# Optimization experiments

Measured on AMD Instinct MI355X. Metric: run time of the kernel, lower is better.

Reference implementation:

```python
import jax, jax.numpy as jnp
import numpy as np

B, C, H, W = 4, 192, 64, 64
D_STATE, D_CONV, EXPAND = 16, 4, 2
DIN = EXPAND * C            # 384
DT_RANK = (C + 15) // 16    # 12
EPS = 1e-5


def _silu(v):
    return v * jax.nn.sigmoid(v)


def _snake(x2d):
    # x2d: [B, H, W, D]; reverse every odd row (boustrophedon / snake scan).
    # This op is its own inverse.
    odd = (jnp.arange(x2d.shape[1]) % 2 == 1)[None, :, None, None]
    return jnp.where(odd, jnp.flip(x2d, axis=2), x2d)


def setup_inputs() -> dict:
    key = jax.random.key(0)
    ks = jax.random.split(key, 12)
    s = lambda k, shape, sc: jax.random.normal(k, shape, dtype=jnp.float32) * sc
    inp = {
        "x": jax.random.normal(ks[0], (B, C, H, W), dtype=jnp.float32),
        "gn_gamma": jnp.ones((C,), jnp.float32),
        "gn_beta": jnp.zeros((C,), jnp.float32),
        "in_proj_w": s(ks[1], (2 * DIN, C), 0.05),
        "conv1d_w": s(ks[2], (DIN, D_CONV), 0.2),
        "conv1d_b": jnp.zeros((DIN,), jnp.float32),
        "x_proj_w": s(ks[3], (DT_RANK + 2 * D_STATE, DIN), 0.05),
        "dt_proj_w": s(ks[4], (DIN, DT_RANK), 0.1),
        "dt_proj_b": s(ks[5], (DIN,), 0.1),
        "A_log": jnp.log(jnp.broadcast_to(jnp.arange(1, D_STATE + 1, dtype=jnp.float32), (DIN, D_STATE))),
        "Dskip": jnp.ones((DIN,), jnp.float32),
        "le_w": s(ks[6], (DIN, 1, 3, 3), 0.1),      # depthwise 3x3 local enhancement
        "out_proj_w": s(ks[7], (C, DIN), 0.05),
        "proj_out_w": s(ks[8], (C, C), 0.05),        # 1x1 conv, no bias
    }
    return inp


def reference(x, gn_gamma, gn_beta, in_proj_w, conv1d_w, conv1d_b,
              x_proj_w, dt_proj_w, dt_proj_b, A_log, Dskip, le_w,
              out_proj_w, proj_out_w):
    b, c, h, w = x.shape
    L = h * w
    din = DIN

    # GroupNorm(1, C): normalize over (C, H, W) per sample
    mu = jnp.mean(x, axis=(1, 2, 3), keepdims=True)
    var = jnp.var(x, axis=(1, 2, 3), keepdims=True)
    xn = (x - mu) * jax.lax.rsqrt(var + EPS)
    xn = xn * gn_gamma[None, :, None, None] + gn_beta[None, :, None, None]

    xs = xn.reshape(b, c, L).transpose(0, 2, 1)            # [B, L, C]

    # input projection -> (u, z)
    xz = jnp.einsum('blc,dc->bld', xs, in_proj_w)          # [B, L, 2*din]
    u, z = jnp.split(xz, 2, axis=-1)

    # snake scan ordering on u
    u = _snake(u.reshape(b, h, w, din)).reshape(b, L, din)

    # causal depthwise conv1d along sequence + SiLU
    u_t = u.transpose(0, 2, 1)                              # [B, din, L]
    u_c = jax.lax.conv_general_dilated(
        u_t, conv1d_w[:, None, :], (1,), [(D_CONV - 1, 0)],
        feature_group_count=din)
    u_c = _silu(u_c + conv1d_b[None, :, None]).transpose(0, 2, 1)  # [B, L, din]

    # input-dependent SSM parameters
    dbl = jnp.einsum('bld,ed->ble', u_c, x_proj_w)          # [B, L, dt_rank+2N]
    dt, Bm, Cm = jnp.split(dbl, [DT_RANK, DT_RANK + D_STATE], axis=-1)
    delta = jax.nn.softplus(jnp.einsum('blr,dr->bld', dt, dt_proj_w) + dt_proj_b)
    A = -jnp.exp(A_log)                                     # [din, N]

    # selective scan over L steps, carry state [B, din, N]
    def step(hc, inp):
        d_t, B_t, C_t, u_t_ = inp                           # [B,din],[B,N],[B,N],[B,din]
        dA = jnp.exp(d_t[..., None] * A)                    # [B, din, N]
        hc = dA * hc + (d_t * u_t_)[..., None] * B_t[:, None, :]
        y_t = jnp.einsum('bdn,bn->bd', hc, C_t)
        return hc, y_t

    h0 = jnp.zeros((b, din, D_STATE), delta.dtype)
    xs_scan = (delta.transpose(1, 0, 2), Bm.transpose(1, 0, 2),
               Cm.transpose(1, 0, 2), u_c.transpose(1, 0, 2))
    _, ys = jax.lax.scan(step, h0, xs_scan)                 # ys: [L, B, din]
    y = ys.transpose(1, 0, 2) + u_c * Dskip                 # [B, L, din]

    # undo snake ordering (involution), then gate with z (raster order)
    y = _snake(y.reshape(b, h, w, din)).reshape(b, L, din)
    y = y * _silu(z)

    # local enhancement: depthwise 3x3 conv residual on the 2D map
    y2d = y.reshape(b, h, w, din).transpose(0, 3, 1, 2)     # [B, din, H, W]
    y_le = jax.lax.conv_general_dilated(
        y2d, le_w, (1, 1), [(1, 1), (1, 1)], feature_group_count=din)
    y = y + y_le.transpose(0, 2, 3, 1).reshape(b, L, din)

    # output projection back to C, reshape, then 1x1 conv
    out_seq = jnp.einsum('bld,cd->blc', y, out_proj_w)      # [B, L, C]
    out = out_seq.transpose(0, 2, 1).reshape(b, c, h, w)
    out = jnp.einsum('bchw,oc->bohw', out, proj_out_w)
    return out
```

## Files before the change

kernel.cpp:

```cpp
#include <hip/hip_runtime.h>
#include <cstddef>

constexpr int CB  = 4;
constexpr int CC  = 192;
constexpr int CH  = 64;
constexpr int CW  = 64;
constexpr int CL  = CH * CW;
constexpr int DIN = 384;
constexpr int NST = 16;
constexpr int DTR = 12;

constexpr int NCHUNK = 64;
constexpr int NELEM  = CB * DIN * NST;

constexpr int WS_PART  = 0;
constexpr int WS_STAT  = 512;
constexpr int WS_BFIN  = 1024;
constexpr int WS_BFOUT = WS_BFIN + 73728;
constexpr int WS_BFPO  = WS_BFOUT + 36864;
constexpr int WS_BFXF  = WS_BFPO + 18432;
constexpr int WS_LWT   = WS_BFXF + 86016;
constexpr int WS_BIG   = WS_LWT + 3456;
constexpr size_t NBL   = (size_t)CB * CL;
constexpr size_t BIGSZ = NBL * DIN;

using half8 = __attribute__((ext_vector_type(8))) _Float16;
using half4 = __attribute__((ext_vector_type(4))) _Float16;
using f32x4 = __attribute__((ext_vector_type(4))) float;

__device__ __forceinline__ float sigm(float v) { return 1.f / (1.f + __expf(-v)); }
__device__ __forceinline__ float silu_f(float v) { return v * sigm(v); }
__device__ __forceinline__ float softplus_f(float v) { return v > 20.f ? v : log1pf(__expf(v)); }
template <int PAT>
__device__ __forceinline__ float quadswz(float v) {
  return __int_as_float(__builtin_amdgcn_ds_swizzle(__float_as_int(v), PAT));
}

__global__ __launch_bounds__(256) void gn_partial(const float* __restrict__ x,
                                                  float* __restrict__ part) {
  int b = blockIdx.x >> 6;
  int chunk = blockIdx.x & 63;
  const float* px = x + (size_t)b * CC * CL + (size_t)chunk * 12288;
  float s = 0.f, s2 = 0.f;
  for (int i = threadIdx.x; i < 12288 / 4; i += 256) {
    float4 v = ((const float4*)px)[i];
    s  += v.x + v.y + v.z + v.w;
    s2 += v.x * v.x + v.y * v.y + v.z * v.z + v.w * v.w;
  }
  __shared__ float ls[4], ls2[4];
  for (int off = 32; off; off >>= 1) { s += __shfl_down(s, off); s2 += __shfl_down(s2, off); }
  int wid = threadIdx.x >> 6, lane = threadIdx.x & 63;
  if (lane == 0) { ls[wid] = s; ls2[wid] = s2; }
  __syncthreads();
  if (threadIdx.x == 0) {
    float t = 0.f, t2 = 0.f;
    for (int i = 0; i < 4; i++) { t += ls[i]; t2 += ls2[i]; }
    part[blockIdx.x * 2] = t;
    part[blockIdx.x * 2 + 1] = t2;
  }
}

__global__ __launch_bounds__(256) void gn_final(const float* __restrict__ part,
                                                float* __restrict__ stat) {
  int b = threadIdx.x >> 6;
  int i = threadIdx.x & 63;
  float s = part[(b * 64 + i) * 2];
  float s2 = part[(b * 64 + i) * 2 + 1];
  for (int off = 32; off; off >>= 1) { s += __shfl_down(s, off); s2 += __shfl_down(s2, off); }
  if (i == 0) {
    float n = (float)(CC * CL);
    float mu = s / n;
    float var = s2 / n - mu * mu;
    stat[b * 2] = mu;
    stat[b * 2 + 1] = rsqrtf(var + 1e-5f);
  }
}

__device__ __forceinline__ void pack_frag(_Float16* dst, int idx, int KS,
                                          const float* __restrict__ W, int KDIM) {
  int j = idx & 7, lane = (idx >> 3) & 63, colq = (idx >> 9) & 3, rest = idx >> 11;
  int ks = rest % KS, nt = rest / KS;
  int col = nt * 64 + colq * 16 + (lane & 15);
  int k = ks * 32 + ((lane >> 4) << 3) + j;
  dst[idx] = (_Float16)W[(size_t)col * KDIM + k];
}

__device__ __forceinline__ void pack_xf(_Float16* dst, int idx,
                                        const float* __restrict__ xw,
                                        const float* __restrict__ dtw) {
  int j = idx & 7, lane = (idx >> 3) & 63, colq = (idx >> 9) & 3, rest = idx >> 11;
  int ks = rest % 12, nt = rest / 12;
  int col = nt * 64 + colq * 16 + (lane & 15);
  int k = ks * 32 + ((lane >> 4) << 3) + j;
  float v = 0.f;
  if (col < 384) {
#pragma unroll
    for (int r = 0; r < 12; r++)
      v += xw[r * 384 + k] * dtw[col * 12 + r];
  } else if (col < 416) {
    v = xw[(col - 384 + 12) * 384 + k];
  }
  dst[idx] = (_Float16)v;
}

__global__ __launch_bounds__(256) void transpose_all(
    const float* __restrict__ in_proj_w, const float* __restrict__ x_proj_w,
    const float* __restrict__ dt_proj_w, const float* __restrict__ out_proj_w,
    const float* __restrict__ proj_out_w, const float* __restrict__ le_w,
    float* __restrict__ ws) {
  int idx = blockIdx.x * 256 + threadIdx.x;
  if (idx < 147456) {
    pack_frag((_Float16*)(ws + WS_BFIN), idx, 6, in_proj_w, 192);
    return;
  }
  idx -= 147456;
  if (idx < 73728) {
    pack_frag((_Float16*)(ws + WS_BFOUT), idx, 12, out_proj_w, 384);
    return;
  }
  idx -= 73728;
  if (idx < 36864) {
    pack_frag((_Float16*)(ws + WS_BFPO), idx, 6, proj_out_w, 192);
    return;
  }
  idx -= 36864;
  if (idx < 172032) {
    pack_xf((_Float16*)(ws + WS_BFXF), idx, x_proj_w, dt_proj_w);
    return;
  }
  idx -= 172032;
  if (idx < 3456) {
    int t9 = idx / 384, d = idx % 384;
    ws[WS_LWT + idx] = le_w[d * 9 + t9];
  }
}

__global__ __launch_bounds__(256) void gemm_inproj_mfma(
    const float* __restrict__ x, const _Float16* __restrict__ Bf,
    const float* __restrict__ stat, const float* __restrict__ gamma,
    const float* __restrict__ beta, float* __restrict__ u, float* __restrict__ z) {
  int mt = blockIdx.x & 255, nt = blockIdx.x >> 8;
  int m0 = mt * 64;
  int b = m0 >> 12, l0 = m0 & 4095;
  float mu = stat[b * 2], rs = stat[b * 2 + 1];
  __shared__ __align__(16) _Float16 Ah[64][200];
  int tid = threadIdx.x;
  int row = tid & 63, cq = tid >> 6;
#pragma unroll
  for (int i = 0; i < 12; i++) {
    int c0 = cq * 4 + i * 16;
    half4 h;
#pragma unroll
    for (int cc = 0; cc < 4; cc++) {
      int c = c0 + cc;
      float g = gamma[c] * rs;
      float bt = beta[c] - mu * g;
      float xv = x[((size_t)(b * 192 + c) << 12) + l0 + row];
      h[cc] = (_Float16)(xv * g + bt);
    }
    *(half4*)&Ah[row][c0] = h;
  }
  __syncthreads();
  int w = tid >> 6, lane = tid & 63;
  int wm = (w >> 1) * 32, wcol = w & 1;
  int r16 = lane & 15, kg = lane >> 4;
  f32x4 acc[2][2] = {};
#pragma unroll
  for (int ks = 0; ks < 6; ks++) {
    half8 a0 = *(const half8*)&Ah[wm + r16][ks * 32 + kg * 8];
    half8 a1 = *(const half8*)&Ah[wm + 16 + r16][ks * 32 + kg * 8];
    half8 b0 = *(const half8*)&Bf[(((size_t)(nt * 6 + ks) * 4 + wcol * 2 + 0) << 9) + lane * 8];
    half8 b1 = *(const half8*)&Bf[(((size_t)(nt * 6 + ks) * 4 + wcol * 2 + 1) << 9) + lane * 8];
    acc[0][0] = __builtin_amdgcn_mfma_f32_16x16x32_f16(a0, b0, acc[0][0], 0, 0, 0);
    acc[0][1] = __builtin_amdgcn_mfma_f32_16x16x32_f16(a0, b1, acc[0][1], 0, 0, 0);
    acc[1][0] = __builtin_amdgcn_mfma_f32_16x16x32_f16(a1, b0, acc[1][0], 0, 0, 0);
    acc[1][1] = __builtin_amdgcn_mfma_f32_16x16x32_f16(a1, b1, acc[1][1], 0, 0, 0);
  }
  int hrow = l0 >> 6;
  bool odd = hrow & 1;
#pragma unroll
  for (int mi = 0; mi < 2; mi++)
#pragma unroll
    for (int ni = 0; ni < 2; ni++)
#pragma unroll
      for (int r = 0; r < 4; r++) {
        int wloc = wm + mi * 16 + kg * 4 + r;
        int d = nt * 64 + wcol * 32 + ni * 16 + r16;
        float val = acc[mi][ni][r];
        if (d < DIN) {
          int ls = odd ? (hrow << 6) + 63 - wloc : l0 + wloc;
          u[((size_t)(b << 12) + ls) * DIN + d] = val;
        } else {
          z[((size_t)(b << 12) + l0 + wloc) * DIN + (d - DIN)] = val;
        }
      }
}

template <int KDIM, int NDIM, bool TRANSOUT>
__global__ __launch_bounds__(256) void gemm_mfma(
    const float* __restrict__ A, const _Float16* __restrict__ Bf,
    float* __restrict__ C) {
  constexpr int KS = KDIM / 32;
  int mt = blockIdx.x & 255, nt = blockIdx.x >> 8;
  int m0 = mt * 64, n0 = nt * 64;
  __shared__ __align__(16) _Float16 Ah[64][KDIM + 8];
  int tid = threadIdx.x;
  {
    int r16s = tid >> 4, kq = tid & 15;
#pragma unroll
    for (int rr = 0; rr < 4; rr++) {
      int rowi = r16s + rr * 16;
#pragma unroll
      for (int kk = 0; kk < KDIM / 64; kk++) {
        float4 v = *(const float4*)&A[(size_t)(m0 + rowi) * KDIM + kk * 64 + kq * 4];
        half4 h;
        h[0] = (_Float16)v.x; h[1] = (_Float16)v.y;
        h[2] = (_Float16)v.z; h[3] = (_Float16)v.w;
        *(half4*)&Ah[rowi][kk * 64 + kq * 4] = h;
      }
    }
  }
  __syncthreads();
  int w = tid >> 6, lane = tid & 63;
  int wm = (w >> 1) * 32, wcol = w & 1;
  int r16 = lane & 15, kg = lane >> 4;
  f32x4 acc[2][2] = {};
#pragma unroll
  for (int ks = 0; ks < KS; ks++) {
    half8 a0 = *(const half8*)&Ah[wm + r16][ks * 32 + kg * 8];
    half8 a1 = *(const half8*)&Ah[wm + 16 + r16][ks * 32 + kg * 8];
    half8 b0 = *(const half8*)&Bf[(((size_t)(nt * KS + ks) * 4 + wcol * 2 + 0) << 9) + lane * 8];
    half8 b1 = *(const half8*)&Bf[(((size_t)(nt * KS + ks) * 4 + wcol * 2 + 1) << 9) + lane * 8];
    acc[0][0] = __builtin_amdgcn_mfma_f32_16x16x32_f16(a0, b0, acc[0][0], 0, 0, 0);
    acc[0][1] = __builtin_amdgcn_mfma_f32_16x16x32_f16(a0, b1, acc[0][1], 0, 0, 0);
    acc[1][0] = __builtin_amdgcn_mfma_f32_16x16x32_f16(a1, b0, acc[1][0], 0, 0, 0);
    acc[1][1] = __builtin_amdgcn_mfma_f32_16x16x32_f16(a1, b1, acc[1][1], 0, 0, 0);
  }
  if constexpr (!TRANSOUT) {
#pragma unroll
    for (int mi = 0; mi < 2; mi++)
#pragma unroll
      for (int ni = 0; ni < 2; ni++)
#pragma unroll
        for (int r = 0; r < 4; r++) {
          int rowo = wm + mi * 16 + kg * 4 + r;
          int col = wcol * 32 + ni * 16 + r16;
          C[(size_t)(m0 + rowo) * NDIM + n0 + col] = acc[mi][ni][r];
        }
  } else {
    __shared__ float Cs[64][68];
#pragma unroll
    for (int mi = 0; mi < 2; mi++)
#pragma unroll
      for (int ni = 0; ni < 2; ni++)
#pragma unroll
        for (int r = 0; r < 4; r++)
          Cs[wcol * 32 + ni * 16 + r16][wm + mi * 16 + kg * 4 + r] = acc[mi][ni][r];
    __syncthreads();
    int b = m0 >> 12, l0 = m0 & 4095;
    int li = tid & 63;
#pragma unroll
    for (int rr = 0; rr < 16; rr++) {
      int o = rr * 4 + (tid >> 6);
      C[(size_t)(b * CC + n0 + o) * CL + l0 + li] = Cs[o][li];
    }
  }
}

__global__ __launch_bounds__(256) void xfull_gemm(
    const float* __restrict__ uc, const _Float16* __restrict__ Bf,
    const float* __restrict__ dt_bias, float* __restrict__ delta,
    float* __restrict__ Bmb, float* __restrict__ Cmb) {
  int mt = blockIdx.x & 255, nt = blockIdx.x >> 8;
  int m0 = mt * 64;
  __shared__ __align__(16) _Float16 Ah[64][392];
  int tid = threadIdx.x;
  {
    int r16s = tid >> 4, kq = tid & 15;
#pragma unroll
    for (int rr = 0; rr < 4; rr++) {
      int rowi = r16s + rr * 16;
#pragma unroll
      for (int kk = 0; kk < 6; kk++) {
        float4 v = *(const float4*)&uc[(size_t)(m0 + rowi) * DIN + kk * 64 + kq * 4];
        half4 h;
        h[0] = (_Float16)v.x; h[1] = (_Float16)v.y;
        h[2] = (_Float16)v.z; h[3] = (_Float16)v.w;
        *(half4*)&Ah[rowi][kk * 64 + kq * 4] = h;
      }
    }
  }
  __syncthreads();
  int w = tid >> 6, lane = tid & 63;
  int wm = (w >> 1) * 32, wcol = w & 1;
  int r16 = lane & 15, kg = lane >> 4;
  f32x4 acc[2][2] = {};
#pragma unroll
  for (int ks = 0; ks < 12; ks++) {
    half8 a0 = *(const half8*)&Ah[wm + r16][ks * 32 + kg * 8];
    half8 a1 = *(const half8*)&Ah[wm + 16 + r16][ks * 32 + kg * 8];
    half8 b0 = *(const half8*)&Bf[(((size_t)(nt * 12 + ks) * 4 + wcol * 2 + 0) << 9) + lane * 8];
    half8 b1 = *(const half8*)&Bf[(((size_t)(nt * 12 + ks) * 4 + wcol * 2 + 1) << 9) + lane * 8];
    acc[0][0] = __builtin_amdgcn_mfma_f32_16x16x32_f16(a0, b0, acc[0][0], 0, 0, 0);
    acc[0][1] = __builtin_amdgcn_mfma_f32_16x16x32_f16(a0, b1, acc[0][1], 0, 0, 0);
    acc[1][0] = __builtin_amdgcn_mfma_f32_16x16x32_f16(a1, b0, acc[1][0], 0, 0, 0);
    acc[1][1] = __builtin_amdgcn_mfma_f32_16x16x32_f16(a1, b1, acc[1][1], 0, 0, 0);
  }
#pragma unroll
  for (int mi = 0; mi < 2; mi++)
#pragma unroll
    for (int ni = 0; ni < 2; ni++)
#pragma unroll
      for (int r = 0; r < 4; r++) {
        size_t m = m0 + wm + mi * 16 + kg * 4 + r;
        int gc = nt * 64 + wcol * 32 + ni * 16 + r16;
        float val = acc[mi][ni][r];
        if (gc < 384)
          delta[m * DIN + gc] = softplus_f(val + dt_bias[gc]);
        else if (gc < 400)
          Bmb[m * 16 + (gc - 384)] = val;
        else if (gc < 416)
          Cmb[m * 16 + (gc - 400)] = val;
      }
}

__global__ __launch_bounds__(256) void conv_silu_tiled(
    const float* __restrict__ u, const float* __restrict__ cw,
    const float* __restrict__ cb, float* __restrict__ uc) {
  int bid = blockIdx.x;
  int dg = bid % 6;
  int lt = (bid / 6) % 64;
  int b  = bid / (6 * 64);
  int d0 = dg * 64;
  int l0 = lt * 64;
  __shared__ float S[67][68];
  int t = threadIdx.x;
  for (int idx = t; idx < 67 * 16; idx += 256) {
    int row = idx >> 4, c4i = idx & 15;
    int l = l0 + row - 3;
    float4 v = make_float4(0.f, 0.f, 0.f, 0.f);
    if (l >= 0)
      v = *(const float4*)&u[((size_t)((b << 12) + l)) * DIN + d0 + c4i * 4];
    *(float4*)&S[row][c4i * 4] = v;
  }
  __syncthreads();
  int c4 = t & 15, j0 = (t >> 4) << 2;
  int dd = d0 + c4 * 4;
  float4 cwv[4];
#pragma unroll
  for (int i = 0; i < 4; i++) cwv[i] = *(const float4*)&cw[(dd + i) * 4];
  float4 bias = *(const float4*)&cb[dd];
  float4 win[7];
#pragma unroll
  for (int k = 0; k < 7; k++) win[k] = *(float4*)&S[j0 + k][c4 * 4];
#pragma unroll
  for (int j = 0; j < 4; j++) {
    float4 acc = bias;
#pragma unroll
    for (int k = 0; k < 4; k++) {
      float4 v = win[j + k];
      acc.x = fmaf(v.x, ((const float*)&cwv[0])[k], acc.x);
      acc.y = fmaf(v.y, ((const float*)&cwv[1])[k], acc.y);
      acc.z = fmaf(v.z, ((const float*)&cwv[2])[k], acc.z);
      acc.w = fmaf(v.w, ((const float*)&cwv[3])[k], acc.w);
    }
    acc.x = silu_f(acc.x);
    acc.y = silu_f(acc.y);
    acc.z = silu_f(acc.z);
    acc.w = silu_f(acc.w);
    *(float4*)&uc[((size_t)((b << 12) + l0 + j0 + j)) * DIN + dd] = acc;
  }
}

__global__ __launch_bounds__(256) void scan_partial(
    const float* __restrict__ delta, const float* __restrict__ uc,
    const float* __restrict__ Bmb, const float* __restrict__ A_log,
    float* __restrict__ hend, float* __restrict__ Pbuf) {
  int bid = blockIdx.x;
  int chunk = bid & 63, bg = bid >> 6;
  int b = bg / 6, g = bg % 6;
  int t = threadIdx.x;
  int dloc = t >> 2, q = t & 3;
  int d = g * 64 + dloc;
  __shared__ float sD[64][64], sU[64][64], sB[64][16];
  size_t baseBL = ((size_t)b << 12) + chunk * 64;
  {
    int row = t >> 2, cg = (t & 3) * 16;
    const float* dp = &delta[(baseBL + row) * DIN + g * 64 + cg];
    const float* up = &uc[(baseBL + row) * DIN + g * 64 + cg];
#pragma unroll
    for (int c = 0; c < 4; c++) {
      *(float4*)&sD[row][cg + 4 * c] = *(const float4*)&dp[4 * c];
      *(float4*)&sU[row][cg + 4 * c] = *(const float4*)&up[4 * c];
    }
    *(float4*)&sB[row][q * 4] = *(const float4*)&Bmb[(baseBL + row) * 16 + q * 4];
  }
  __syncthreads();
  float4 av = *(const float4*)&A_log[d * 16 + 4 * q];
  float a0 = -__expf(av.x), a1 = -__expf(av.y), a2 = -__expf(av.z), a3 = -__expf(av.w);
  float h0 = 0.f, h1 = 0.f, h2 = 0.f, h3 = 0.f, sdel = 0.f;
#pragma unroll 8
  for (int ll = 0; ll < 64; ll++) {
    float dv = sD[ll][dloc];
    float uv = sU[ll][dloc];
    float4 Bv = *(const float4*)&sB[ll][q * 4];
    float duv = dv * uv;
    h0 = fmaf(__expf(dv * a0), h0, duv * Bv.x);
    h1 = fmaf(__expf(dv * a1), h1, duv * Bv.y);
    h2 = fmaf(__expf(dv * a2), h2, duv * Bv.z);
    h3 = fmaf(__expf(dv * a3), h3, duv * Bv.w);
    sdel += dv;
  }
  size_t e = ((size_t)(b * DIN + d)) * 16 + 4 * q;
  float4 hv; hv.x = h0; hv.y = h1; hv.z = h2; hv.w = h3;
  *(float4*)&hend[(size_t)chunk * NELEM + e] = hv;
  float4 pv;
  pv.x = __expf(a0 * sdel); pv.y = __expf(a1 * sdel);
  pv.z = __expf(a2 * sdel); pv.w = __expf(a3 * sdel);
  *(float4*)&Pbuf[(size_t)chunk * NELEM + e] = pv;
}

__global__ __launch_bounds__(256) void scan_combine(
    const float* __restrict__ hend, const float* __restrict__ Pbuf,
    float* __restrict__ hin) {
  int e = blockIdx.x * 256 + threadIdx.x;
  float h = 0.f;
  float Pc = Pbuf[e], Hc = hend[e];
#pragma unroll 8
  for (int c = 0; c < NCHUNK; c++) {
    float Pn = 0.f, Hn = 0.f;
    if (c < NCHUNK - 1) {
      Pn = Pbuf[(size_t)(c + 1) * NELEM + e];
      Hn = hend[(size_t)(c + 1) * NELEM + e];
    }
    hin[(size_t)c * NELEM + e] = h;
    h = fmaf(Pc, h, Hc);
    Pc = Pn; Hc = Hn;
  }
}

__global__ __launch_bounds__(256) void scan_final(
    const float* __restrict__ delta, const float* __restrict__ uc,
    const float* __restrict__ Bmb, const float* __restrict__ Cmb,
    const float* __restrict__ A_log, const float* __restrict__ Dskip,
    const float* __restrict__ z, const float* __restrict__ hin,
    float* __restrict__ yr) {
  int bid = blockIdx.x;
  int chunk = bid & 63, bg = bid >> 6;
  int b = bg / 6, g = bg % 6;
  int t = threadIdx.x;
  int dloc = t >> 2, q = t & 3;
  int d = g * 64 + dloc;
  __shared__ float sD[64][64], sU[64][64], sB[64][16], sC[64][16];
  size_t baseBL = ((size_t)b << 12) + chunk * 64;
  {
    int row = t >> 2, cg = (t & 3) * 16;
    const float* dp = &delta[(baseBL + row) * DIN + g * 64 + cg];
    const float* up = &uc[(baseBL + row) * DIN + g * 64 + cg];
#pragma unroll
    for (int c = 0; c < 4; c++) {
      *(float4*)&sD[row][cg + 4 * c] = *(const float4*)&dp[4 * c];
      *(float4*)&sU[row][cg + 4 * c] = *(const float4*)&up[4 * c];
    }
    *(float4*)&sB[row][q * 4] = *(const float4*)&Bmb[(baseBL + row) * 16 + q * 4];
    *(float4*)&sC[row][q * 4] = *(const float4*)&Cmb[(baseBL + row) * 16 + q * 4];
  }
  __syncthreads();
  float4 av = *(const float4*)&A_log[d * 16 + 4 * q];
  float a0 = -__expf(av.x), a1 = -__expf(av.y), a2 = -__expf(av.z), a3 = -__expf(av.w);
  size_t e = ((size_t)(b * DIN + d)) * 16 + 4 * q;
  float4 hv = *(const float4*)&hin[(size_t)chunk * NELEM + e];
  float h0 = hv.x, h1 = hv.y, h2 = hv.z, h3 = hv.w;
  float yk[16];
#pragma unroll
  for (int ll = 0; ll < 64; ll++) {
    float dv = sD[ll][dloc];
    float uv = sU[ll][dloc];
    float4 Bv = *(const float4*)&sB[ll][q * 4];
    float4 Cv = *(const float4*)&sC[ll][q * 4];
    float duv = dv * uv;
    h0 = fmaf(__expf(dv * a0), h0, duv * Bv.x);
    h1 = fmaf(__expf(dv * a1), h1, duv * Bv.y);
    h2 = fmaf(__expf(dv * a2), h2, duv * Bv.z);
    h3 = fmaf(__expf(dv * a3), h3, duv * Bv.w);
    float yp = h0 * Cv.x + h1 * Cv.y + h2 * Cv.z + h3 * Cv.w;
    yp += quadswz<0x041F>(yp);
    yp += quadswz<0x081F>(yp);
    if ((ll & 3) == q) yk[ll >> 2] = yp;
  }
  float dsk = Dskip[d];
  bool odd = chunk & 1;
#pragma unroll
  for (int i = 0; i < 16; i++) {
    int ll = 4 * i + q;
    int wr = odd ? 63 - ll : ll;
    size_t ro = baseBL + wr;
    float uvll = sU[ll][dloc];
    float zv = z[ro * DIN + d];
    yr[ro * DIN + d] = (yk[i] + uvll * dsk) * silu_f(zv);
  }
}

__global__ __launch_bounds__(256) void le_conv_tiled(
    const float* __restrict__ yr, const float* __restrict__ lwT,
    float* __restrict__ y2) {
  int bid = blockIdx.x;
  int dg = bid % 24;
  int ht = (bid / 24) % 16;
  int b  = bid / (24 * 16);
  int d0 = dg * 16;
  int h0 = ht * 4;
  __shared__ float S[6][66][20];
  int t = threadIdx.x;
  int dq = t & 3, w = t >> 2;
#pragma unroll
  for (int r = 0; r < 6; r++) {
    int hh = h0 - 1 + r;
    float4 v = make_float4(0.f, 0.f, 0.f, 0.f);
    if (hh >= 0 && hh < 64)
      v = *(const float4*)&yr[((size_t)((b << 12) + (hh << 6) + w)) * DIN + d0 + dq * 4];
    *(float4*)&S[r][w + 1][dq * 4] = v;
    if (w == 0)  *(float4*)&S[r][0][dq * 4]  = make_float4(0.f, 0.f, 0.f, 0.f);
    if (w == 63) *(float4*)&S[r][65][dq * 4] = make_float4(0.f, 0.f, 0.f, 0.f);
  }
  __syncthreads();
  float4 wv[9];
#pragma unroll
  for (int i = 0; i < 9; i++)
    wv[i] = *(const float4*)&lwT[i * DIN + d0 + dq * 4];
#pragma unroll
  for (int hr = 0; hr < 4; hr++) {
    float4 acc = *(float4*)&S[hr + 1][w + 1][dq * 4];
#pragma unroll
    for (int ki = 0; ki < 3; ki++)
#pragma unroll
      for (int kj = 0; kj < 3; kj++) {
        float4 v = *(float4*)&S[hr + ki][w + kj][dq * 4];
        float4 c = wv[ki * 3 + kj];
        acc.x = fmaf(v.x, c.x, acc.x);
        acc.y = fmaf(v.y, c.y, acc.y);
        acc.z = fmaf(v.z, c.z, acc.z);
        acc.w = fmaf(v.w, c.w, acc.w);
      }
    int l = ((h0 + hr) << 6) + w;
    *(float4*)&y2[((size_t)((b << 12) + l)) * DIN + d0 + dq * 4] = acc;
  }
}

extern "C" void kernel_launch(void* const* d_in, const int* in_sizes, int n_in,
                              void* d_out, int out_size, void* d_ws, size_t ws_size,
                              hipStream_t stream) {
  const float* x          = (const float*)d_in[0];
  const float* gn_gamma   = (const float*)d_in[1];
  const float* gn_beta    = (const float*)d_in[2];
  const float* in_proj_w  = (const float*)d_in[3];
  const float* conv1d_w   = (const float*)d_in[4];
  const float* conv1d_b   = (const float*)d_in[5];
  const float* x_proj_w   = (const float*)d_in[6];
  const float* dt_proj_w  = (const float*)d_in[7];
  const float* dt_proj_b  = (const float*)d_in[8];
  const float* A_log      = (const float*)d_in[9];
  const float* Dskip      = (const float*)d_in[10];
  const float* le_w       = (const float*)d_in[11];
  const float* out_proj_w = (const float*)d_in[12];
  const float* proj_out_w = (const float*)d_in[13];
  float* out = (float*)d_out;

  float* ws      = (float*)d_ws;
  float* part    = ws + WS_PART;
  float* stat    = ws + WS_STAT;
  _Float16* BfIn  = (_Float16*)(ws + WS_BFIN);
  _Float16* BfOut = (_Float16*)(ws + WS_BFOUT);
  _Float16* BfPo  = (_Float16*)(ws + WS_BFPO);
  _Float16* BfXf  = (_Float16*)(ws + WS_BFXF);
  float* lwT    = ws + WS_LWT;
  float* u      = ws + WS_BIG;
  float* zb     = u + BIGSZ;
  float* uc     = zb + BIGSZ;
  float* delta  = uc + BIGSZ;
  float* yr     = delta + BIGSZ;
  float* Bmb    = yr + BIGSZ;
  float* Cmb    = Bmb + NBL * NST;
  float* y2     = uc;
  float* outseq = u;
  float* hend   = u;
  float* Pbuf   = u + (size_t)NCHUNK * NELEM;
  float* hin    = u + 2 * (size_t)NCHUNK * NELEM;

  gn_partial<<<256, 256, 0, stream>>>(x, part);
  gn_final<<<1, 256, 0, stream>>>(part, stat);
  transpose_all<<<1694, 256, 0, stream>>>(in_proj_w, x_proj_w, dt_proj_w,
                                          out_proj_w, proj_out_w, le_w, ws);
  gemm_inproj_mfma<<<256 * 12, 256, 0, stream>>>(x, BfIn, stat, gn_gamma, gn_beta, u, zb);
  conv_silu_tiled<<<1536, 256, 0, stream>>>(u, conv1d_w, conv1d_b, uc);
  xfull_gemm<<<256 * 7, 256, 0, stream>>>(uc, BfXf, dt_proj_b, delta, Bmb, Cmb);
  scan_partial<<<1536, 256, 0, stream>>>(delta, uc, Bmb, A_log, hend, Pbuf);
  scan_combine<<<96, 256, 0, stream>>>(hend, Pbuf, hin);
  scan_final<<<1536, 256, 0, stream>>>(delta, uc, Bmb, Cmb, A_log, Dskip,
                                       zb, hin, yr);
  le_conv_tiled<<<1536, 256, 0, stream>>>(yr, lwT, y2);
  gemm_mfma<384, 192, false><<<256 * 3, 256, 0, stream>>>(y2, BfOut, outseq);
  gemm_mfma<192, 192, true><<<256 * 3, 256, 0, stream>>>(outseq, BfPo, out);
}
```

Measured before the change: 269.9 us.

## Emit fp16 MFMA-fragment-layout activations from producers and feed GEMMs directly

The conv_silu and local-enhancement kernels now write fp16 copies of their outputs laid out in the MFMA A-fragment order. The x_proj, out_proj and proj_out GEMMs then load A operands straight from global memory with no LDS staging or fp32-to-fp16 conversion. The out_proj GEMM writes its result as fp16 fragments for the final GEMM, which halves intermediate traffic. The cost is an extra fp16 store in conv_silu and the loss of A-tile reuse across waves within a block, which now rely on cache.

```diff
diff --git a/kernel.cpp b/kernel.cpp
--- a/kernel.cpp
+++ b/kernel.cpp
@@ -34,6 +34,12 @@
 template <int PAT>
 __device__ __forceinline__ float quadswz(float v) {
   return __int_as_float(__builtin_amdgcn_ds_swizzle(__float_as_int(v), PAT));
+}
+
+__device__ __forceinline__ size_t afrag_idx(int m, int k, int KS) {
+  int m16 = m >> 4, r16 = m & 15;
+  int ks = k >> 5, kg = (k & 31) >> 3, j = k & 7;
+  return (((size_t)(m16 * KS + ks)) << 9) + (size_t)(((kg << 4) + r16) << 3) + j;
 }
 
 __global__ __launch_bounds__(256) void gn_partial(const float* __restrict__ x,
@@ -196,109 +202,22 @@
       }
 }
 
-template <int KDIM, int NDIM, bool TRANSOUT>
-__global__ __launch_bounds__(256) void gemm_mfma(
-    const float* __restrict__ A, const _Float16* __restrict__ Bf,
-    float* __restrict__ C) {
-  constexpr int KS = KDIM / 32;
-  int mt = blockIdx.x & 255, nt = blockIdx.x >> 8;
-  int m0 = mt * 64, n0 = nt * 64;
-  __shared__ __align__(16) _Float16 Ah[64][KDIM + 8];
-  int tid = threadIdx.x;
-  {
-    int r16s = tid >> 4, kq = tid & 15;
-#pragma unroll
-    for (int rr = 0; rr < 4; rr++) {
-      int rowi = r16s + rr * 16;
-#pragma unroll
-      for (int kk = 0; kk < KDIM / 64; kk++) {
-        float4 v = *(const float4*)&A[(size_t)(m0 + rowi) * KDIM + kk * 64 + kq * 4];
-        half4 h;
-        h[0] = (_Float16)v.x; h[1] = (_Float16)v.y;
-        h[2] = (_Float16)v.z; h[3] = (_Float16)v.w;
-        *(half4*)&Ah[rowi][kk * 64 + kq * 4] = h;
-      }
-    }
-  }
-  __syncthreads();
-  int w = tid >> 6, lane = tid & 63;
-  int wm = (w >> 1) * 32, wcol = w & 1;
-  int r16 = lane & 15, kg = lane >> 4;
-  f32x4 acc[2][2] = {};
-#pragma unroll
-  for (int ks = 0; ks < KS; ks++) {
-    half8 a0 = *(const half8*)&Ah[wm + r16][ks * 32 + kg * 8];
-    half8 a1 = *(const half8*)&Ah[wm + 16 + r16][ks * 32 + kg * 8];
-    half8 b0 = *(const half8*)&Bf[(((size_t)(nt * KS + ks) * 4 + wcol * 2 + 0) << 9) + lane * 8];
-    half8 b1 = *(const half8*)&Bf[(((size_t)(nt * KS + ks) * 4 + wcol * 2 + 1) << 9) + lane * 8];
-    acc[0][0] = __builtin_amdgcn_mfma_f32_16x16x32_f16(a0, b0, acc[0][0], 0, 0, 0);
-    acc[0][1] = __builtin_amdgcn_mfma_f32_16x16x32_f16(a0, b1, acc[0][1], 0, 0, 0);
-    acc[1][0] = __builtin_amdgcn_mfma_f32_16x16x32_f16(a1, b0, acc[1][0], 0, 0, 0);
-    acc[1][1] = __builtin_amdgcn_mfma_f32_16x16x32_f16(a1, b1, acc[1][1], 0, 0, 0);
-  }
-  if constexpr (!TRANSOUT) {
-#pragma unroll
-    for (int mi = 0; mi < 2; mi++)
-#pragma unroll
-      for (int ni = 0; ni < 2; ni++)
-#pragma unroll
-        for (int r = 0; r < 4; r++) {
-          int rowo = wm + mi * 16 + kg * 4 + r;
-          int col = wcol * 32 + ni * 16 + r16;
-          C[(size_t)(m0 + rowo) * NDIM + n0 + col] = acc[mi][ni][r];
-        }
-  } else {
-    __shared__ float Cs[64][68];
-#pragma unroll
-    for (int mi = 0; mi < 2; mi++)
-#pragma unroll
-      for (int ni = 0; ni < 2; ni++)
-#pragma unroll
-        for (int r = 0; r < 4; r++)
-          Cs[wcol * 32 + ni * 16 + r16][wm + mi * 16 + kg * 4 + r] = acc[mi][ni][r];
-    __syncthreads();
-    int b = m0 >> 12, l0 = m0 & 4095;
-    int li = tid & 63;
-#pragma unroll
-    for (int rr = 0; rr < 16; rr++) {
-      int o = rr * 4 + (tid >> 6);
-      C[(size_t)(b * CC + n0 + o) * CL + l0 + li] = Cs[o][li];
-    }
-  }
-}
-
-__global__ __launch_bounds__(256) void xfull_gemm(
-    const float* __restrict__ uc, const _Float16* __restrict__ Bf,
+__global__ __launch_bounds__(256) void xfull_direct(
+    const _Float16* __restrict__ Af, const _Float16* __restrict__ Bf,
     const float* __restrict__ dt_bias, float* __restrict__ delta,
     float* __restrict__ Bmb, float* __restrict__ Cmb) {
   int mt = blockIdx.x & 255, nt = blockIdx.x >> 8;
   int m0 = mt * 64;
-  __shared__ __align__(16) _Float16 Ah[64][392];
   int tid = threadIdx.x;
-  {
-    int r16s = tid >> 4, kq = tid & 15;
-#pragma unroll
-    for (int rr = 0; rr < 4; rr++) {
-      int rowi = r16s + rr * 16;
-#pragma unroll
-      for (int kk = 0; kk < 6; kk++) {
-        float4 v = *(const float4*)&uc[(size_t)(m0 + rowi) * DIN + kk * 64 + kq * 4];
-        half4 h;
-        h[0] = (_Float16)v.x; h[1] = (_Float16)v.y;
-        h[2] = (_Float16)v.z; h[3] = (_Float16)v.w;
-        *(half4*)&Ah[rowi][kk * 64 + kq * 4] = h;
-      }
-    }
-  }
-  __syncthreads();
   int w = tid >> 6, lane = tid & 63;
   int wm = (w >> 1) * 32, wcol = w & 1;
   int r16 = lane & 15, kg = lane >> 4;
+  int m16a = (m0 + wm) >> 4;
   f32x4 acc[2][2] = {};
 #pragma unroll
   for (int ks = 0; ks < 12; ks++) {
-    half8 a0 = *(const half8*)&Ah[wm + r16][ks * 32 + kg * 8];
-    half8 a1 = *(const half8*)&Ah[wm + 16 + r16][ks * 32 + kg * 8];
+    half8 a0 = *(const half8*)&Af[(((size_t)(m16a * 12 + ks)) << 9) + lane * 8];
+    half8 a1 = *(const half8*)&Af[(((size_t)((m16a + 1) * 12 + ks)) << 9) + lane * 8];
     half8 b0 = *(const half8*)&Bf[(((size_t)(nt * 12 + ks) * 4 + wcol * 2 + 0) << 9) + lane * 8];
     half8 b1 = *(const half8*)&Bf[(((size_t)(nt * 12 + ks) * 4 + wcol * 2 + 1) << 9) + lane * 8];
     acc[0][0] = __builtin_amdgcn_mfma_f32_16x16x32_f16(a0, b0, acc[0][0], 0, 0, 0);
@@ -324,9 +243,98 @@
       }
 }
 
+__global__ __launch_bounds__(256) void gemm_out_direct(
+    const _Float16* __restrict__ Af, const _Float16* __restrict__ Bf,
+    _Float16* __restrict__ outh) {
+  int mt = blockIdx.x & 255, nt = blockIdx.x >> 8;
+  int m0 = mt * 64;
+  int tid = threadIdx.x;
+  int w = tid >> 6, lane = tid & 63;
+  int wm = (w >> 1) * 32, wcol = w & 1;
+  int r16 = lane & 15, kg = lane >> 4;
+  int m16a = (m0 + wm) >> 4;
+  f32x4 acc[2][2] = {};
+#pragma unroll
+  for (int ks = 0; ks < 12; ks++) {
+    half8 a0 = *(const half8*)&Af[(((size_t)(m16a * 12 + ks)) << 9) + lane * 8];
+    half8 a1 = *(const half8*)&Af[(((size_t)((m16a + 1) * 12 + ks)) << 9) + lane * 8];
+    half8 b0 = *(const half8*)&Bf[(((size_t)(nt * 12 + ks) * 4 + wcol * 2 + 0) << 9) + lane * 8];
+    half8 b1 = *(const half8*)&Bf[(((size_t)(nt * 12 + ks) * 4 + wcol * 2 + 1) << 9) + lane * 8];
+    acc[0][0] = __builtin_amdgcn_mfma_f32_16x16x32_f16(a0, b0, acc[0][0], 0, 0, 0);
+    acc[0][1] = __builtin_amdgcn_mfma_f32_16x16x32_f16(a0, b1, acc[0][1], 0, 0, 0);
+    acc[1][0] = __builtin_amdgcn_mfma_f32_16x16x32_f16(a1, b0, acc[1][0], 0, 0, 0);
+    acc[1][1] = __builtin_amdgcn_mfma_f32_16x16x32_f16(a1, b1, acc[1][1], 0, 0, 0);
+  }
+  __shared__ float Cs[64][69];
+#pragma unroll
+  for (int mi = 0; mi < 2; mi++)
+#pragma unroll
+    for (int ni = 0; ni < 2; ni++)
+#pragma unroll
+      for (int r = 0; r < 4; r++)
+        Cs[wm + mi * 16 + kg * 4 + r][wcol * 32 + ni * 16 + r16] = acc[mi][ni][r];
+  __syncthreads();
+  int pair = tid >> 5, l32 = tid & 31;
+  int mi2 = pair >> 1, ksl = pair & 1;
+#pragma unroll
+  for (int it = 0; it < 2; it++) {
+    int lane2 = l32 + it * 32;
+    int r16b = lane2 & 15, kgb = lane2 >> 4;
+    int rowl = mi2 * 16 + r16b;
+    int coll = ksl * 32 + kgb * 8;
+    half8 h;
+#pragma unroll
+    for (int jj = 0; jj < 8; jj++) h[jj] = (_Float16)Cs[rowl][coll + jj];
+    size_t m16o = (size_t)((m0 >> 4) + mi2);
+    int kso = nt * 2 + ksl;
+    *(half8*)&outh[((m16o * 6 + kso) << 9) + lane2 * 8] = h;
+  }
+}
+
+__global__ __launch_bounds__(256) void gemm_po_direct(
+    const _Float16* __restrict__ Af, const _Float16* __restrict__ Bf,
+    float* __restrict__ C) {
+  int mt = blockIdx.x & 255, nt = blockIdx.x >> 8;
+  int m0 = mt * 64, n0 = nt * 64;
+  int tid = threadIdx.x;
+  int w = tid >> 6, lane = tid & 63;
+  int wm = (w >> 1) * 32, wcol = w & 1;
+  int r16 = lane & 15, kg = lane >> 4;
+  int m16a = (m0 + wm) >> 4;
+  f32x4 acc[2][2] = {};
+#pragma unroll
+  for (int ks = 0; ks < 6; ks++) {
+    half8 a0 = *(const half8*)&Af[(((size_t)(m16a * 6 + ks)) << 9) + lane * 8];
+    half8 a1 = *(const half8*)&Af[(((size_t)((m16a + 1) * 6 + ks)) << 9) + lane * 8];
+    half8 b0 = *(const half8*)&Bf[(((size_t)(nt * 6 + ks) * 4 + wcol * 2 + 0) << 9) + lane * 8];
+    half8 b1 = *(const half8*)&Bf[(((size_t)(nt * 6 + ks) * 4 + wcol * 2 + 1) << 9) + lane * 8];
+    acc[0][0] = __builtin_amdgcn_mfma_f32_16x16x32_f16(a0, b0, acc[0][0], 0, 0, 0);
+    acc[0][1] = __builtin_amdgcn_mfma_f32_16x16x32_f16(a0, b1, acc[0][1], 0, 0, 0);
+    acc[1][0] = __builtin_amdgcn_mfma_f32_16x16x32_f16(a1, b0, acc[1][0], 0, 0, 0);
+    acc[1][1] = __builtin_amdgcn_mfma_f32_16x16x32_f16(a1, b1, acc[1][1], 0, 0, 0);
+  }
+  __shared__ float Cs[64][69];
+#pragma unroll
+  for (int mi = 0; mi < 2; mi++)
+#pragma unroll
+    for (int ni = 0; ni < 2; ni++)
+#pragma unroll
+      for (int r = 0; r < 4; r++)
+        Cs[wcol * 32 + ni * 16 + r16][wm + mi * 16 + kg * 4 + r] = acc[mi][ni][r];
+  __syncthreads();
+  int b = m0 >> 12, l0 = m0 & 4095;
+  int li = tid & 63;
+#pragma unroll
+  for (int rr = 0; rr < 16; rr++) {
+    int o = rr * 4 + (tid >> 6);
+    C[(size_t)(b * CC + n0 + o) * CL + l0 + li] = Cs[o][li];
+  }
+}
+
 __global__ __launch_bounds__(256) void conv_silu_tiled(
     const float* __restrict__ u, const float* __restrict__ cw,
-    const float* __restrict__ cb, float* __restrict__ uc) {
+    const float* __restrict__ cb, float* __restrict__ uc,
+    _Float16* __restrict__ uc_h) {
   int bid = blockIdx.x;
   int dg = bid % 6;
   int lt = (bid / 6) % 64;
@@ -368,7 +376,13 @@
     acc.y = silu_f(acc.y);
     acc.z = silu_f(acc.z);
     acc.w = silu_f(acc.w);
-    *(float4*)&uc[((size_t)((b << 12) + l0 + j0 + j)) * DIN + dd] = acc;
+    int l = l0 + j0 + j;
+    int m = (b << 12) + l;
+    *(float4*)&uc[(size_t)m * DIN + dd] = acc;
+    half4 h;
+    h[0] = (_Float16)acc.x; h[1] = (_Float16)acc.y;
+    h[2] = (_Float16)acc.z; h[3] = (_Float16)acc.w;
+    *(half4*)&uc_h[afrag_idx(m, dd, 12)] = h;
   }
 }
 
@@ -503,14 +517,14 @@
 
 __global__ __launch_bounds__(256) void le_conv_tiled(
     const float* __restrict__ yr, const float* __restrict__ lwT,
-    float* __restrict__ y2) {
+    _Float16* __restrict__ y2h) {
   int bid = blockIdx.x;
   int dg = bid % 24;
   int ht = (bid / 24) % 16;
   int b  = bid / (24 * 16);
   int d0 = dg * 16;
   int h0 = ht * 4;
-  __shared__ float S[6][66][20];
+  __shared__ float S[6][66][24];
   int t = threadIdx.x;
   int dq = t & 3, w = t >> 2;
 #pragma unroll
@@ -543,7 +557,11 @@
         acc.w = fmaf(v.w, c.w, acc.w);
       }
     int l = ((h0 + hr) << 6) + w;
-    *(float4*)&y2[((size_t)((b << 12) + l)) * DIN + d0 + dq * 4] = acc;
+    int m = (b << 12) + l;
+    half4 h;
+    h[0] = (_Float16)acc.x; h[1] = (_Float16)acc.y;
+    h[2] = (_Float16)acc.z; h[3] = (_Float16)acc.w;
+    *(half4*)&y2h[afrag_idx(m, d0 + dq * 4, 12)] = h;
   }
 }
 
@@ -581,8 +599,9 @@
   float* yr     = delta + BIGSZ;
   float* Bmb    = yr + BIGSZ;
   float* Cmb    = Bmb + NBL * NST;
-  float* y2     = uc;
-  float* outseq = u;
+  _Float16* uc_h = (_Float16*)yr;
+  _Float16* y2h  = (_Float16*)delta;
+  _Float16* outh = (_Float16*)zb;
   float* hend   = u;
   float* Pbuf   = u + (size_t)NCHUNK * NELEM;
   float* hin    = u + 2 * (size_t)NCHUNK * NELEM;
@@ -592,13 +611,13 @@
   transpose_all<<<1694, 256, 0, stream>>>(in_proj_w, x_proj_w, dt_proj_w,
                                           out_proj_w, proj_out_w, le_w, ws);
   gemm_inproj_mfma<<<256 * 12, 256, 0, stream>>>(x, BfIn, stat, gn_gamma, gn_beta, u, zb);
-  conv_silu_tiled<<<1536, 256, 0, stream>>>(u, conv1d_w, conv1d_b, uc);
-  xfull_gemm<<<256 * 7, 256, 0, stream>>>(uc, BfXf, dt_proj_b, delta, Bmb, Cmb);
+  conv_silu_tiled<<<1536, 256, 0, stream>>>(u, conv1d_w, conv1d_b, uc, uc_h);
+  xfull_direct<<<256 * 7, 256, 0, stream>>>(uc_h, BfXf, dt_proj_b, delta, Bmb, Cmb);
   scan_partial<<<1536, 256, 0, stream>>>(delta, uc, Bmb, A_log, hend, Pbuf);
   scan_combine<<<96, 256, 0, stream>>>(hend, Pbuf, hin);
   scan_final<<<1536, 256, 0, stream>>>(delta, uc, Bmb, Cmb, A_log, Dskip,
                                        zb, hin, yr);
-  le_conv_tiled<<<1536, 256, 0, stream>>>(yr, lwT, y2);
-  gemm_mfma<384, 192, false><<<256 * 3, 256, 0, stream>>>(y2, BfOut, outseq);
-  gemm_mfma<192, 192, true><<<256 * 3, 256, 0, stream>>>(outseq, BfPo, out);
-}
+  le_conv_tiled<<<1536, 256, 0, stream>>>(yr, lwT, y2h);
+  gemm_out_direct<<<256 * 3, 256, 0, stream>>>(y2h, BfOut, outh);
+  gemm_po_direct<<<256 * 3, 256, 0, stream>>>(outh, BfPo, out);
+}
```

Result: faster. 261.9 us (-3.0%).
